# Optimization experiments

Measured on AMD Instinct MI355X. Metric: run time of the kernel, lower is better.

## Reference

```python
import jax, jax.numpy as jnp
import numpy as np

N_POINTS = 500_000
D_PHASE = 6
N_BINS = 128
LO, HI = -4.0, 4.0


def setup_inputs() -> dict:
    key = jax.random.key(0)
    x = jax.random.normal(key, (N_POINTS, D_PHASE), dtype=jnp.float32)
    edges_x = jnp.linspace(LO, HI, N_BINS + 1, dtype=jnp.float32)
    edges_y = jnp.linspace(LO, HI, N_BINS + 1, dtype=jnp.float32)
    return {"x": x, "edges_x": edges_x, "edges_y": edges_y}


def reference(x, edges_x, edges_y):
    # Histogram2D(axis=(0,1), bandwidth=(1.0,1.0), kde=True).forward(x)
    # bin centers from edges
    cx = 0.5 * (edges_x[:-1] + edges_x[1:])  # (nx,)
    cy = 0.5 * (edges_y[:-1] + edges_y[1:])  # (ny,)
    # resolution = first bin width; bandwidth = 1.0 * resolution
    bwx = edges_x[1] - edges_x[0]
    bwy = edges_y[1] - edges_y[0]
    # per-point Gaussian kernel evaluations against bin centers
    kx = jnp.exp(-0.5 * jnp.square((x[:, 0][:, None] - cx[None, :]) / bwx))  # (n, nx)
    ky = jnp.exp(-0.5 * jnp.square((x[:, 1][:, None] - cy[None, :]) / bwy))  # (n, ny)
    # accumulate joint KDE histogram via outer-product contraction over points
    hist = jnp.einsum("ni,nj->ij", kx, ky)  # (nx, ny)
    # normalize to a probability density (integrates to 1 over the grid)
    hist = hist / (jnp.sum(hist) * bwx * bwy)
    return hist
```

## Files before the change

### kernel.cpp

```cpp
#include <hip/hip_runtime.h>

#define NBINS 128
#define NB2   (NBINS * NBINS)
#define TPB   1024
#define NBLK  256
#define KC    64
#define NTEAM 4

typedef __attribute__((ext_vector_type(8)))  short short8;
typedef __attribute__((ext_vector_type(16))) float f32x16;

__device__ __forceinline__ float exp2_fast(float x) {
#if defined(__has_builtin)
#if __has_builtin(__builtin_amdgcn_exp2f)
    return __builtin_amdgcn_exp2f(x);
#else
    return exp2f(x);
#endif
#else
    return exp2f(x);
#endif
}

__device__ __forceinline__ unsigned pk_bf16(float a, float b) {
    const unsigned ar = __float_as_uint(a) + 0x8000u;
    const unsigned br = __float_as_uint(b) + 0x8000u;
    return __builtin_amdgcn_perm(br, ar, 0x07060302u);
}

#define WC (-0.72134752044448170f)

union S8 { short8 s; unsigned u[4]; };

__global__ __launch_bounds__(TPB, 4) void kde_mfma_kernel(
    const float* __restrict__ x,
    const float* __restrict__ ex,
    const float* __restrict__ ey,
    float* __restrict__ out,
    int n, int nchunks)
{
    __shared__ float hist[NB2];
    __shared__ __align__(16) float u_s[2][NTEAM][KC];
    __shared__ __align__(16) float v_s[2][NTEAM][KC];

    const int tid  = (int)threadIdx.x;
    const int lane = tid & 63;
    const int half = lane >> 5;
    const int l31  = lane & 31;
    const int w4   = (tid >> 6) & 3;
    const int team = tid >> 8;
    const int rowblk = (w4 >> 1) * 64;
    const int colblk = (w4 & 1) * 64;
    const float rowf = (float)(rowblk + l31);
    const float colf = (float)(colblk + l31);

    const float lox = ex[0], loy = ey[0];
    const float ibx = 1.0f / (ex[1] - ex[0]);
    const float iby = 1.0f / (ey[1] - ey[0]);

    f32x16 acc[2][2];
    #pragma unroll
    for (int a = 0; a < 2; ++a)
        #pragma unroll
        for (int c = 0; c < 2; ++c)
            #pragma unroll
            for (int r = 0; r < 16; ++r) acc[a][c][r] = 0.f;

    auto stage = [&](int it, int bb) {
        if (tid < NTEAM * KC) {
            const int tm  = tid >> 6, idx = tid & 63;
            const int g   = (int)blockIdx.x * NTEAM + tm + it * (NBLK * NTEAM);
            if (g < nchunks) {
                const int p = g * KC + idx;
                float uu = 1e9f, vv = 1e9f;
                if (p < n) {
                    const float2 xy = *(const float2*)(x + (size_t)p * 6);
                    uu = (xy.x - lox) * ibx - 0.5f;
                    vv = (xy.y - loy) * iby - 0.5f;
                }
                u_s[bb][tm][idx] = uu; v_s[bb][tm][idx] = vv;
            }
        }
    };

    const int niter = (nchunks + NBLK * NTEAM - 1) / (NBLK * NTEAM);
    stage(0, 0);
    for (int it = 0; it < niter; ++it) {
        __syncthreads();
        if (it + 1 < niter) stage(it + 1, (it + 1) & 1);
        const int bb = it & 1;
        const int g = (int)blockIdx.x * NTEAM + team + it * (NBLK * NTEAM);
        if (g < nchunks) {
            const float* us = u_s[bb][team];
            const float* vs = v_s[bb][team];
            #pragma unroll
            for (int s4 = 0; s4 < 4; ++s4) {
                const int kb = s4 * 16 + half * 8;
                const float4 ua = *(const float4*)&us[kb];
                const float4 ub = *(const float4*)&us[kb + 4];
                const float4 va = *(const float4*)&vs[kb];
                const float4 vb = *(const float4*)&vs[kb + 4];

                S8 af[2], bf[2];
                #pragma unroll
                for (int rb = 0; rb < 2; ++rb) {
                    const float m = rowf + (float)(rb * 32);
                    float d0 = ua.x - m, d1 = ua.y - m, d2 = ua.z - m, d3 = ua.w - m;
                    float d4 = ub.x - m, d5 = ub.y - m, d6 = ub.z - m, d7 = ub.w - m;
                    const float w0 = exp2_fast((WC * d0) * d0);
                    const float w1 = exp2_fast((WC * d1) * d1);
                    const float w2 = exp2_fast((WC * d2) * d2);
                    const float w3 = exp2_fast((WC * d3) * d3);
                    const float w4f = exp2_fast((WC * d4) * d4);
                    const float w5 = exp2_fast((WC * d5) * d5);
                    const float w6 = exp2_fast((WC * d6) * d6);
                    const float w7 = exp2_fast((WC * d7) * d7);
                    af[rb].u[0] = pk_bf16(w0, w1);
                    af[rb].u[1] = pk_bf16(w2, w3);
                    af[rb].u[2] = pk_bf16(w4f, w5);
                    af[rb].u[3] = pk_bf16(w6, w7);
                }
                #pragma unroll
                for (int tj = 0; tj < 2; ++tj) {
                    const float c = colf + (float)(tj * 32);
                    float d0 = va.x - c, d1 = va.y - c, d2 = va.z - c, d3 = va.w - c;
                    float d4 = vb.x - c, d5 = vb.y - c, d6 = vb.z - c, d7 = vb.w - c;
                    const float w0 = exp2_fast((WC * d0) * d0);
                    const float w1 = exp2_fast((WC * d1) * d1);
                    const float w2 = exp2_fast((WC * d2) * d2);
                    const float w3 = exp2_fast((WC * d3) * d3);
                    const float w4f = exp2_fast((WC * d4) * d4);
                    const float w5 = exp2_fast((WC * d5) * d5);
                    const float w6 = exp2_fast((WC * d6) * d6);
                    const float w7 = exp2_fast((WC * d7) * d7);
                    bf[tj].u[0] = pk_bf16(w0, w1);
                    bf[tj].u[1] = pk_bf16(w2, w3);
                    bf[tj].u[2] = pk_bf16(w4f, w5);
                    bf[tj].u[3] = pk_bf16(w6, w7);
                }
                #pragma unroll
                for (int rb = 0; rb < 2; ++rb)
                    #pragma unroll
                    for (int tj = 0; tj < 2; ++tj)
                        acc[rb][tj] = __builtin_amdgcn_mfma_f32_32x32x16_bf16(
                            af[rb].s, bf[tj].s, acc[rb][tj], 0, 0, 0);
            }
        }
    }
    __syncthreads();

    for (int tm = 0; tm < NTEAM; ++tm) {
        if (team == tm) {
            #pragma unroll
            for (int rb = 0; rb < 2; ++rb)
                #pragma unroll
                for (int tj = 0; tj < 2; ++tj)
                    #pragma unroll
                    for (int r = 0; r < 16; ++r) {
                        const int row = rowblk + rb * 32 + (r & 3) + 8 * (r >> 2) + 4 * half;
                        const int col = colblk + tj * 32 + l31;
                        const int a = row * NBINS + col;
                        const float v = acc[rb][tj][r];
                        if (tm == 0) hist[a] = v;
                        else         hist[a] += v;
                    }
        }
        __syncthreads();
    }

    for (int i = tid; i < NB2; i += TPB)
        unsafeAtomicAdd(&out[i], hist[i]);
}

__global__ __launch_bounds__(TPB) void kde_final_kernel(
    float* __restrict__ out,
    const float* __restrict__ ex,
    const float* __restrict__ ey)
{
    __shared__ float red[TPB / 64];
    __shared__ float sinv;
    const int tid = (int)threadIdx.x;

    float4 v[4];
    float s = 0.f;
    #pragma unroll
    for (int i = 0; i < 4; ++i) {
        v[i] = ((const float4*)out)[tid + i * TPB];
        s += v[i].x + v[i].y + v[i].z + v[i].w;
    }
    #pragma unroll
    for (int off = 32; off > 0; off >>= 1) s += __shfl_down(s, off, 64);
    if ((tid & 63) == 0) red[tid >> 6] = s;
    __syncthreads();
    if (tid == 0) {
        float t = 0.f;
        #pragma unroll
        for (int i = 0; i < TPB / 64; ++i) t += red[i];
        sinv = 1.0f / (t * (ex[1] - ex[0]) * (ey[1] - ey[0]));
    }
    __syncthreads();
    const float inv = sinv;
    #pragma unroll
    for (int i = 0; i < 4; ++i) {
        float4 o = v[i];
        o.x *= inv; o.y *= inv; o.z *= inv; o.w *= inv;
        ((float4*)out)[tid + i * TPB] = o;
    }
}

extern "C" void kernel_launch(void* const* d_in, const int* in_sizes, int n_in,
                              void* d_out, int out_size, void* d_ws, size_t ws_size,
                              hipStream_t stream)
{
    const float* x  = (const float*)d_in[0];
    const float* ex = (const float*)d_in[1];
    const float* ey = (const float*)d_in[2];
    float* out = (float*)d_out;
    const int n = in_sizes[0] / 6;
    const int nchunks = (n + KC - 1) / KC;

    hipMemsetAsync(d_out, 0, NB2 * sizeof(float), stream);
    kde_mfma_kernel<<<NBLK, TPB, 0, stream>>>(x, ex, ey, out, n, nchunks);
    kde_final_kernel<<<1, TPB, 0, stream>>>(out, ex, ey);
}
```

Before: 126.4 us.

## Give each wave the full 128x128 tile and fuse normalization via last-block counter

Each wave now computes the entire 128x128 histogram tile (4x4 MFMA accumulators) for its own 64-point chunk, so every kernel weight is computed once per point instead of being duplicated across waves that each covered a quadrant. Blocks shrink to 256 threads with per-wave staging loaded straight from registers, which removes the per-iteration block-wide barrier. The separate normalization kernel is replaced by a last-block-done atomic counter in workspace, saving one launch. In exchange, each thread holds 256 accumulator registers, which limits occupancy, and a second workspace memset is added.

```diff
diff --git a/kernel.cpp b/kernel.cpp
--- a/kernel.cpp
+++ b/kernel.cpp
@@ -2,25 +2,12 @@
 
 #define NBINS 128
 #define NB2   (NBINS * NBINS)
-#define TPB   1024
+#define TPB   256
 #define NBLK  256
 #define KC    64
-#define NTEAM 4
 
 typedef __attribute__((ext_vector_type(8)))  short short8;
 typedef __attribute__((ext_vector_type(16))) float f32x16;
-
-__device__ __forceinline__ float exp2_fast(float x) {
-#if defined(__has_builtin)
-#if __has_builtin(__builtin_amdgcn_exp2f)
-    return __builtin_amdgcn_exp2f(x);
-#else
-    return exp2f(x);
-#endif
-#else
-    return exp2f(x);
-#endif
-}
 
 __device__ __forceinline__ unsigned pk_bf16(float a, float b) {
     const unsigned ar = __float_as_uint(a) + 0x8000u;
@@ -32,179 +19,159 @@
 
 union S8 { short8 s; unsigned u[4]; };
 
-__global__ __launch_bounds__(TPB, 4) void kde_mfma_kernel(
+__device__ __forceinline__ S8 gen_frag(const float4 a, const float4 b, float base) {
+    float d0 = a.x - base, d1 = a.y - base, d2 = a.z - base, d3 = a.w - base;
+    float d4 = b.x - base, d5 = b.y - base, d6 = b.z - base, d7 = b.w - base;
+    const float w0 = __builtin_amdgcn_exp2f((WC * d0) * d0);
+    const float w1 = __builtin_amdgcn_exp2f((WC * d1) * d1);
+    const float w2 = __builtin_amdgcn_exp2f((WC * d2) * d2);
+    const float w3 = __builtin_amdgcn_exp2f((WC * d3) * d3);
+    const float w4 = __builtin_amdgcn_exp2f((WC * d4) * d4);
+    const float w5 = __builtin_amdgcn_exp2f((WC * d5) * d5);
+    const float w6 = __builtin_amdgcn_exp2f((WC * d6) * d6);
+    const float w7 = __builtin_amdgcn_exp2f((WC * d7) * d7);
+    S8 r;
+    r.u[0] = pk_bf16(w0, w1); r.u[1] = pk_bf16(w2, w3);
+    r.u[2] = pk_bf16(w4, w5); r.u[3] = pk_bf16(w6, w7);
+    return r;
+}
+
+__global__ __launch_bounds__(TPB, 1) void kde_mfma_kernel(
     const float* __restrict__ x,
     const float* __restrict__ ex,
     const float* __restrict__ ey,
     float* __restrict__ out,
+    unsigned* __restrict__ counter,
     int n, int nchunks)
 {
     __shared__ float hist[NB2];
-    __shared__ __align__(16) float u_s[2][NTEAM][KC];
-    __shared__ __align__(16) float v_s[2][NTEAM][KC];
+    __shared__ float hist2[NB2];
+    __shared__ __align__(16) float u_s[4][KC];
+    __shared__ __align__(16) float v_s[4][KC];
+    __shared__ float redbuf[4];
+    __shared__ int   lastflag;
 
     const int tid  = (int)threadIdx.x;
     const int lane = tid & 63;
     const int half = lane >> 5;
     const int l31  = lane & 31;
-    const int w4   = (tid >> 6) & 3;
-    const int team = tid >> 8;
-    const int rowblk = (w4 >> 1) * 64;
-    const int colblk = (w4 & 1) * 64;
-    const float rowf = (float)(rowblk + l31);
-    const float colf = (float)(colblk + l31);
+    const int wave = tid >> 6;
+    const float l31f = (float)l31;
 
     const float lox = ex[0], loy = ey[0];
     const float ibx = 1.0f / (ex[1] - ex[0]);
     const float iby = 1.0f / (ey[1] - ey[0]);
 
-    f32x16 acc[2][2];
+    f32x16 acc[4][4];
     #pragma unroll
-    for (int a = 0; a < 2; ++a)
+    for (int a = 0; a < 4; ++a)
         #pragma unroll
-        for (int c = 0; c < 2; ++c)
+        for (int c = 0; c < 4; ++c)
             #pragma unroll
             for (int r = 0; r < 16; ++r) acc[a][c][r] = 0.f;
 
-    auto stage = [&](int it, int bb) {
-        if (tid < NTEAM * KC) {
-            const int tm  = tid >> 6, idx = tid & 63;
-            const int g   = (int)blockIdx.x * NTEAM + tm + it * (NBLK * NTEAM);
-            if (g < nchunks) {
-                const int p = g * KC + idx;
-                float uu = 1e9f, vv = 1e9f;
-                if (p < n) {
-                    const float2 xy = *(const float2*)(x + (size_t)p * 6);
-                    uu = (xy.x - lox) * ibx - 0.5f;
-                    vv = (xy.y - loy) * iby - 0.5f;
-                }
-                u_s[bb][tm][idx] = uu; v_s[bb][tm][idx] = vv;
+    const int gstep = NBLK * 4;
+    int g = (int)blockIdx.x * 4 + wave;
+
+    float uu = 1e9f, vv = 1e9f;
+    {
+        const int p = g * KC + lane;
+        if (g < nchunks && p < n) {
+            const float2 xy = *(const float2*)(x + (size_t)p * 6);
+            uu = (xy.x - lox) * ibx - 0.5f;
+            vv = (xy.y - loy) * iby - 0.5f;
+        }
+    }
+
+    for (; g < nchunks; g += gstep) {
+        u_s[wave][lane] = uu; v_s[wave][lane] = vv;
+
+        const int gn = g + gstep;
+        uu = 1e9f; vv = 1e9f;
+        if (gn < nchunks) {
+            const int p = gn * KC + lane;
+            if (p < n) {
+                const float2 xy = *(const float2*)(x + (size_t)p * 6);
+                uu = (xy.x - lox) * ibx - 0.5f;
+                vv = (xy.y - loy) * iby - 0.5f;
             }
         }
-    };
 
-    const int niter = (nchunks + NBLK * NTEAM - 1) / (NBLK * NTEAM);
-    stage(0, 0);
-    for (int it = 0; it < niter; ++it) {
-        __syncthreads();
-        if (it + 1 < niter) stage(it + 1, (it + 1) & 1);
-        const int bb = it & 1;
-        const int g = (int)blockIdx.x * NTEAM + team + it * (NBLK * NTEAM);
-        if (g < nchunks) {
-            const float* us = u_s[bb][team];
-            const float* vs = v_s[bb][team];
+        #pragma unroll
+        for (int s4 = 0; s4 < 4; ++s4) {
+            const int kb = s4 * 16 + half * 8;
+            const float4 ua = *(const float4*)&u_s[wave][kb];
+            const float4 ub = *(const float4*)&u_s[wave][kb + 4];
+            const float4 va = *(const float4*)&v_s[wave][kb];
+            const float4 vb = *(const float4*)&v_s[wave][kb + 4];
+
+            S8 af[4], bf[4];
             #pragma unroll
-            for (int s4 = 0; s4 < 4; ++s4) {
-                const int kb = s4 * 16 + half * 8;
-                const float4 ua = *(const float4*)&us[kb];
-                const float4 ub = *(const float4*)&us[kb + 4];
-                const float4 va = *(const float4*)&vs[kb];
-                const float4 vb = *(const float4*)&vs[kb + 4];
-
-                S8 af[2], bf[2];
+            for (int t = 0; t < 4; ++t) {
+                af[t] = gen_frag(ua, ub, l31f + (float)(t * 32));
+                bf[t] = gen_frag(va, vb, l31f + (float)(t * 32));
+            }
+            #pragma unroll
+            for (int rt = 0; rt < 4; ++rt)
                 #pragma unroll
-                for (int rb = 0; rb < 2; ++rb) {
-                    const float m = rowf + (float)(rb * 32);
-                    float d0 = ua.x - m, d1 = ua.y - m, d2 = ua.z - m, d3 = ua.w - m;
-                    float d4 = ub.x - m, d5 = ub.y - m, d6 = ub.z - m, d7 = ub.w - m;
-                    const float w0 = exp2_fast((WC * d0) * d0);
-                    const float w1 = exp2_fast((WC * d1) * d1);
-                    const float w2 = exp2_fast((WC * d2) * d2);
-                    const float w3 = exp2_fast((WC * d3) * d3);
-                    const float w4f = exp2_fast((WC * d4) * d4);
-                    const float w5 = exp2_fast((WC * d5) * d5);
-                    const float w6 = exp2_fast((WC * d6) * d6);
-                    const float w7 = exp2_fast((WC * d7) * d7);
-                    af[rb].u[0] = pk_bf16(w0, w1);
-                    af[rb].u[1] = pk_bf16(w2, w3);
-                    af[rb].u[2] = pk_bf16(w4f, w5);
-                    af[rb].u[3] = pk_bf16(w6, w7);
-                }
-                #pragma unroll
-                for (int tj = 0; tj < 2; ++tj) {
-                    const float c = colf + (float)(tj * 32);
-                    float d0 = va.x - c, d1 = va.y - c, d2 = va.z - c, d3 = va.w - c;
-                    float d4 = vb.x - c, d5 = vb.y - c, d6 = vb.z - c, d7 = vb.w - c;
-                    const float w0 = exp2_fast((WC * d0) * d0);
-                    const float w1 = exp2_fast((WC * d1) * d1);
-                    const float w2 = exp2_fast((WC * d2) * d2);
-                    const float w3 = exp2_fast((WC * d3) * d3);
-                    const float w4f = exp2_fast((WC * d4) * d4);
-                    const float w5 = exp2_fast((WC * d5) * d5);
-                    const float w6 = exp2_fast((WC * d6) * d6);
-                    const float w7 = exp2_fast((WC * d7) * d7);
-                    bf[tj].u[0] = pk_bf16(w0, w1);
-                    bf[tj].u[1] = pk_bf16(w2, w3);
-                    bf[tj].u[2] = pk_bf16(w4f, w5);
-                    bf[tj].u[3] = pk_bf16(w6, w7);
-                }
-                #pragma unroll
-                for (int rb = 0; rb < 2; ++rb)
-                    #pragma unroll
-                    for (int tj = 0; tj < 2; ++tj)
-                        acc[rb][tj] = __builtin_amdgcn_mfma_f32_32x32x16_bf16(
-                            af[rb].s, bf[tj].s, acc[rb][tj], 0, 0, 0);
-            }
+                for (int ct = 0; ct < 4; ++ct)
+                    acc[rt][ct] = __builtin_amdgcn_mfma_f32_32x32x16_bf16(
+                        af[rt].s, bf[ct].s, acc[rt][ct], 0, 0, 0);
         }
     }
+
     __syncthreads();
-
-    for (int tm = 0; tm < NTEAM; ++tm) {
-        if (team == tm) {
+    #pragma unroll
+    for (int ph = 0; ph < 2; ++ph) {
+        if ((wave & 1) == ph) {
+            float* hb = (wave >> 1) ? hist2 : hist;
             #pragma unroll
-            for (int rb = 0; rb < 2; ++rb)
+            for (int rt = 0; rt < 4; ++rt)
                 #pragma unroll
-                for (int tj = 0; tj < 2; ++tj)
+                for (int ct = 0; ct < 4; ++ct)
                     #pragma unroll
                     for (int r = 0; r < 16; ++r) {
-                        const int row = rowblk + rb * 32 + (r & 3) + 8 * (r >> 2) + 4 * half;
-                        const int col = colblk + tj * 32 + l31;
-                        const int a = row * NBINS + col;
-                        const float v = acc[rb][tj][r];
-                        if (tm == 0) hist[a] = v;
-                        else         hist[a] += v;
+                        const int row = rt * 32 + (r & 3) + 8 * (r >> 2) + 4 * half;
+                        const int a = row * NBINS + ct * 32 + l31;
+                        if (ph == 0) hb[a] = acc[rt][ct][r];
+                        else         hb[a] += acc[rt][ct][r];
                     }
         }
         __syncthreads();
     }
 
     for (int i = tid; i < NB2; i += TPB)
-        unsafeAtomicAdd(&out[i], hist[i]);
-}
+        unsafeAtomicAdd(&out[i], hist[i] + hist2[i]);
 
-__global__ __launch_bounds__(TPB) void kde_final_kernel(
-    float* __restrict__ out,
-    const float* __restrict__ ex,
-    const float* __restrict__ ey)
-{
-    __shared__ float red[TPB / 64];
-    __shared__ float sinv;
-    const int tid = (int)threadIdx.x;
-
-    float4 v[4];
-    float s = 0.f;
-    #pragma unroll
-    for (int i = 0; i < 4; ++i) {
-        v[i] = ((const float4*)out)[tid + i * TPB];
-        s += v[i].x + v[i].y + v[i].z + v[i].w;
-    }
-    #pragma unroll
-    for (int off = 32; off > 0; off >>= 1) s += __shfl_down(s, off, 64);
-    if ((tid & 63) == 0) red[tid >> 6] = s;
+    __threadfence();
     __syncthreads();
     if (tid == 0) {
-        float t = 0.f;
-        #pragma unroll
-        for (int i = 0; i < TPB / 64; ++i) t += red[i];
-        sinv = 1.0f / (t * (ex[1] - ex[0]) * (ey[1] - ey[0]));
+        const unsigned old = __hip_atomic_fetch_add(
+            counter, 1u, __ATOMIC_ACQ_REL, __HIP_MEMORY_SCOPE_AGENT);
+        lastflag = (old == (unsigned)(NBLK - 1));
     }
     __syncthreads();
-    const float inv = sinv;
-    #pragma unroll
-    for (int i = 0; i < 4; ++i) {
-        float4 o = v[i];
-        o.x *= inv; o.y *= inv; o.z *= inv; o.w *= inv;
-        ((float4*)out)[tid + i * TPB] = o;
+    if (lastflag) {
+        __threadfence();
+        float4 vals[16];
+        float s = 0.f;
+        #pragma unroll
+        for (int k = 0; k < 16; ++k) {
+            vals[k] = ((const float4*)out)[tid + k * TPB];
+            s += vals[k].x + vals[k].y + vals[k].z + vals[k].w;
+        }
+        #pragma unroll
+        for (int off = 32; off > 0; off >>= 1) s += __shfl_down(s, off, 64);
+        if (lane == 0) redbuf[wave] = s;
+        __syncthreads();
+        const float tot = redbuf[0] + redbuf[1] + redbuf[2] + redbuf[3];
+        const float inv = 1.0f / (tot * (ex[1] - ex[0]) * (ey[1] - ey[0]));
+        #pragma unroll
+        for (int k = 0; k < 16; ++k) {
+            float4 o = vals[k];
+            o.x *= inv; o.y *= inv; o.z *= inv; o.w *= inv;
+            ((float4*)out)[tid + k * TPB] = o;
+        }
     }
 }
 
@@ -220,6 +187,7 @@
     const int nchunks = (n + KC - 1) / KC;
 
     hipMemsetAsync(d_out, 0, NB2 * sizeof(float), stream);
-    kde_mfma_kernel<<<NBLK, TPB, 0, stream>>>(x, ex, ey, out, n, nchunks);
-    kde_final_kernel<<<1, TPB, 0, stream>>>(out, ex, ey);
+    hipMemsetAsync(d_ws, 0, 64, stream);
+    kde_mfma_kernel<<<NBLK, TPB, 0, stream>>>(
+        x, ex, ey, out, (unsigned*)d_ws, n, nchunks);
 }
```

Result: slower. 129.5 us (+2.4%).
